# Optimization experiments

Measured on AMD Instinct MI355X. Metric: run time of the kernel, lower is better.

The kernel has to match this reference:

```python
import jax, jax.numpy as jnp
import numpy as np


def setup_inputs() -> dict:
    key = jax.random.key(0)
    k0, k1, k2, k3, k4 = jax.random.split(key, 5)
    c_in, c_feat, c_atten, T = 256, 256, 64, 8
    b, h, w = 8, 64, 64
    return {
        "x": jax.random.normal(k0, (b * T, c_in, h, w), dtype=jnp.float32),
        "W_feat": jax.random.normal(k1, (c_feat, c_in), dtype=jnp.float32) * 0.02,
        "b_feat": jax.random.normal(k2, (c_feat,), dtype=jnp.float32) * 0.02,
        "W_atten": jax.random.normal(k3, (c_atten, c_in), dtype=jnp.float32) * 0.02,
        "b_atten": jax.random.normal(k4, (c_atten,), dtype=jnp.float32) * 0.02,
        "T": T,
    }


def reference(x, W_feat, b_feat, W_atten, b_atten, T):
    bt, c, h, w = x.shape
    b = bt // T
    hw = h * w
    # first frame of each clip: (b, c, h, w)
    x0 = x.reshape(b, T, c, h, w)[:, 0]
    # 1x1 conv == per-pixel matmul over channels
    feat = jnp.einsum('bchw,fc->bfhw', x0, W_feat) + b_feat[None, :, None, None]
    feat = feat.reshape(b, -1, hw)                      # (b, c_feat, hw)
    atten = jnp.einsum('schw,ac->sahw', x, W_atten) + b_atten[None, :, None, None]
    atten = atten.reshape(b, T * W_atten.shape[0], hw)  # (b, T*c_atten, hw)
    atten = jax.nn.softmax(atten, axis=-1)              # softmax over spatial
    context = jnp.einsum('bfs,bas->bfa', feat, atten)   # (b, c_feat, T*c_atten)
    return (context, atten)
```

## Files before the change

kernel.cpp:

```cpp
#include <hip/hip_runtime.h>
#include <hip/hip_bf16.h>

#define HW    4096
#define CIN   256
#define NB    8
#define T_FR  8
#define CTX_ELEMS (NB * 256 * 512)

typedef __attribute__((ext_vector_type(8))) short short8;
typedef __attribute__((ext_vector_type(4))) float f32x4;

__device__ __forceinline__ unsigned short f2bf(float f) {
  union { float f; unsigned int u; } v; v.f = f;
  unsigned int r = v.u + 0x7fffu + ((v.u >> 16) & 1u);
  return (unsigned short)(r >> 16);
}
__device__ __forceinline__ float bf2f(unsigned short u) {
  union { unsigned int u; float f; } v; v.u = ((unsigned int)u) << 16;
  return v.f;
}

#define LROW 264
__global__ __launch_bounds__(256) void k_feat(
    const float* __restrict__ x, const float* __restrict__ Wf,
    const float* __restrict__ bfeat, unsigned short* __restrict__ featbf) {
  const int p0  = blockIdx.x * 128;
  const int f0t = blockIdx.y * 128;
  const int b   = blockIdx.z;
  __shared__ unsigned short Wsh[128 * LROW];
  const int tid = threadIdx.x, lane = tid & 63, wave = tid >> 6;
  {
    const int row = tid >> 1, seg = tid & 1;
    const float* src = Wf + (size_t)(f0t + row) * CIN + seg * 128;
    unsigned short* dst = &Wsh[row * LROW + seg * 128];
#pragma unroll
    for (int i = 0; i < 16; ++i) {
      float4 va = *(const float4*)(src + i * 8);
      float4 vb = *(const float4*)(src + i * 8 + 4);
      short8 w;
      w[0] = (short)f2bf(va.x); w[1] = (short)f2bf(va.y);
      w[2] = (short)f2bf(va.z); w[3] = (short)f2bf(va.w);
      w[4] = (short)f2bf(vb.x); w[5] = (short)f2bf(vb.y);
      w[6] = (short)f2bf(vb.z); w[7] = (short)f2bf(vb.w);
      *(short8*)(dst + i * 8) = w;
    }
  }
  __syncthreads();
  const int r = lane & 15, kg = lane >> 4;
  const int pw = p0 + wave * 32;
  const float* xs = x + (size_t)(b * T_FR) * CIN * HW;
  f32x4 acc[2][8] = {};
  for (int ks = 0; ks < 8; ++ks) {
    short8 afr[2];
#pragma unroll
    for (int mi = 0; mi < 2; ++mi) {
      const float* col = xs + (size_t)(ks * 32 + kg * 8) * HW + pw + mi * 16 + r;
#pragma unroll
      for (int j = 0; j < 8; ++j) afr[mi][j] = (short)f2bf(col[(size_t)j * HW]);
    }
    short8 bfr[8];
#pragma unroll
    for (int nj = 0; nj < 8; ++nj)
      bfr[nj] = *(const short8*)&Wsh[(nj * 16 + r) * LROW + ks * 32 + kg * 8];
#pragma unroll
    for (int mi = 0; mi < 2; ++mi)
#pragma unroll
      for (int nj = 0; nj < 8; ++nj)
        acc[mi][nj] = __builtin_amdgcn_mfma_f32_16x16x32_bf16(afr[mi], bfr[nj], acc[mi][nj], 0, 0, 0);
  }
#pragma unroll
  for (int nj = 0; nj < 8; ++nj) {
    const int f = f0t + nj * 16 + r;
    const float bias = bfeat[f];
#pragma unroll
    for (int mi = 0; mi < 2; ++mi) {
      ushort4 u;
      u.x = f2bf(acc[mi][nj][0] + bias);
      u.y = f2bf(acc[mi][nj][1] + bias);
      u.z = f2bf(acc[mi][nj][2] + bias);
      u.w = f2bf(acc[mi][nj][3] + bias);
      *(ushort4*)&featbf[(size_t)(b * 256 + f) * HW + pw + mi * 16 + kg * 4] = u;
    }
  }
}

__global__ __launch_bounds__(256) void k_att(
    const float* __restrict__ x, const float* __restrict__ Wa,
    const float* __restrict__ batt, unsigned short* __restrict__ attbf,
    float* __restrict__ rsum_part) {
  const int p0 = blockIdx.x * 128;
  const int s  = blockIdx.y;
  __shared__ unsigned short Wsh[64 * LROW];
  __shared__ float wsum[4][64];
  const int tid = threadIdx.x, lane = tid & 63, wave = tid >> 6;
  {
    const int row = tid >> 2, seg = tid & 3;
    const float* src = Wa + (size_t)row * CIN + seg * 64;
    unsigned short* dst = &Wsh[row * LROW + seg * 64];
#pragma unroll
    for (int i = 0; i < 8; ++i) {
      float4 va = *(const float4*)(src + i * 8);
      float4 vb = *(const float4*)(src + i * 8 + 4);
      short8 w;
      w[0] = (short)f2bf(va.x); w[1] = (short)f2bf(va.y);
      w[2] = (short)f2bf(va.z); w[3] = (short)f2bf(va.w);
      w[4] = (short)f2bf(vb.x); w[5] = (short)f2bf(vb.y);
      w[6] = (short)f2bf(vb.z); w[7] = (short)f2bf(vb.w);
      *(short8*)(dst + i * 8) = w;
    }
  }
  __syncthreads();
  const int r = lane & 15, kg = lane >> 4;
  const int pw = p0 + wave * 32;
  const float* xs = x + (size_t)s * CIN * HW;
  f32x4 acc[2][4] = {};
  for (int ks = 0; ks < 8; ++ks) {
    short8 afr[2];
#pragma unroll
    for (int mi = 0; mi < 2; ++mi) {
      const float* col = xs + (size_t)(ks * 32 + kg * 8) * HW + pw + mi * 16 + r;
#pragma unroll
      for (int j = 0; j < 8; ++j) afr[mi][j] = (short)f2bf(col[(size_t)j * HW]);
    }
    short8 bfr[4];
#pragma unroll
    for (int nj = 0; nj < 4; ++nj)
      bfr[nj] = *(const short8*)&Wsh[(nj * 16 + r) * LROW + ks * 32 + kg * 8];
#pragma unroll
    for (int mi = 0; mi < 2; ++mi)
#pragma unroll
      for (int nj = 0; nj < 4; ++nj)
        acc[mi][nj] = __builtin_amdgcn_mfma_f32_16x16x32_bf16(afr[mi], bfr[nj], acc[mi][nj], 0, 0, 0);
  }
  const int b = s >> 3, t = s & 7;
  float rowpart[4];
#pragma unroll
  for (int nj = 0; nj < 4; ++nj) {
    const int a = nj * 16 + r;
    const float bias = batt[a];
    float sp = 0.f;
#pragma unroll
    for (int mi = 0; mi < 2; ++mi) {
      float e0 = __expf(acc[mi][nj][0] + bias);
      float e1 = __expf(acc[mi][nj][1] + bias);
      float e2 = __expf(acc[mi][nj][2] + bias);
      float e3 = __expf(acc[mi][nj][3] + bias);
      sp += e0 + e1 + e2 + e3;
      ushort4 u;
      u.x = f2bf(e0); u.y = f2bf(e1); u.z = f2bf(e2); u.w = f2bf(e3);
      *(ushort4*)&attbf[(size_t)(b * 512 + t * 64 + a) * HW + pw + mi * 16 + kg * 4] = u;
    }
    sp += __shfl_xor(sp, 16);
    sp += __shfl_xor(sp, 32);
    rowpart[nj] = sp;
  }
  if (lane < 16) {
#pragma unroll
    for (int nj = 0; nj < 4; ++nj) wsum[wave][nj * 16 + r] = rowpart[nj];
  }
  __syncthreads();
  if (tid < 64) {
    float tot = wsum[0][tid] + wsum[1][tid] + wsum[2][tid] + wsum[3][tid];
    rsum_part[(size_t)blockIdx.x * 4096 + b * 512 + t * 64 + tid] = tot;
  }
}

__global__ __launch_bounds__(256) void k_rsum(
    const float* __restrict__ rsum_part, float* __restrict__ rsum) {
  const int row = blockIdx.x * 256 + threadIdx.x;
  float s = 0.f;
#pragma unroll
  for (int j = 0; j < 32; ++j) s += rsum_part[(size_t)j * 4096 + row];
  rsum[row] = s;
}

__global__ __launch_bounds__(256) void k_ctx(
    const unsigned short* __restrict__ featbf,
    const unsigned short* __restrict__ attbf,
    float* __restrict__ partial) {
  const int a0 = blockIdx.x * 64;
  const int ft = blockIdx.y;
  const int b  = blockIdx.z >> 3;
  const int kc = blockIdx.z & 7;
  __shared__ unsigned short Bsh[64 * LROW];
  const int tid = threadIdx.x, lane = tid & 63, wave = tid >> 6;
  const int r = lane & 15, kg = lane >> 4;
  const int fbase = ft * 128 + wave * 32;
  const unsigned short* Arow = featbf + (size_t)(b * 256 + fbase + r) * HW + kc * 512 + kg * 8;
  const unsigned short* Bsrc = attbf + (size_t)(b * 512 + a0 + (tid >> 2)) * HW + kc * 512 + (tid & 3) * 64;
  unsigned short* Bdst = &Bsh[(tid >> 2) * LROW + (tid & 3) * 64];
  f32x4 acc[2][4] = {};
  for (int ch = 0; ch < 2; ++ch) {
    __syncthreads();
#pragma unroll
    for (int i = 0; i < 8; ++i)
      *(short8*)(Bdst + i * 8) = *(const short8*)(Bsrc + ch * 256 + i * 8);
    __syncthreads();
#pragma unroll
    for (int ks = 0; ks < 8; ++ks) {
      short8 afr[2];
      afr[0] = *(const short8*)(Arow + ch * 256 + ks * 32);
      afr[1] = *(const short8*)(Arow + ch * 256 + ks * 32 + (size_t)16 * HW);
      short8 bfr[4];
#pragma unroll
      for (int nj = 0; nj < 4; ++nj)
        bfr[nj] = *(const short8*)&Bsh[(nj * 16 + r) * LROW + ks * 32 + kg * 8];
#pragma unroll
      for (int mi = 0; mi < 2; ++mi)
#pragma unroll
        for (int nj = 0; nj < 4; ++nj)
          acc[mi][nj] = __builtin_amdgcn_mfma_f32_16x16x32_bf16(afr[mi], bfr[nj], acc[mi][nj], 0, 0, 0);
    }
  }
  const size_t base = ((size_t)kc << 20) + (size_t)b * (256 * 512);
#pragma unroll
  for (int mi = 0; mi < 2; ++mi)
#pragma unroll
    for (int nj = 0; nj < 4; ++nj)
#pragma unroll
      for (int reg = 0; reg < 4; ++reg) {
        const int f = fbase + mi * 16 + kg * 4 + reg;
        const int a = a0 + nj * 16 + r;
        partial[base + (size_t)f * 512 + a] = acc[mi][nj][reg];
      }
}

__global__ __launch_bounds__(256) void k_ctxred(
    const float* __restrict__ partial, const float* __restrict__ rsum,
    float* __restrict__ ctx) {
  const int idx = blockIdx.x * 256 + threadIdx.x;
  const int a = idx & 511, b = idx >> 17;
  float s = 0.f;
#pragma unroll
  for (int kc = 0; kc < 8; ++kc) s += partial[((size_t)kc << 20) + idx];
  ctx[idx] = s / rsum[b * 512 + a];
}

__global__ __launch_bounds__(256) void k_attn_out(
    const unsigned short* __restrict__ attbf, const float* __restrict__ rsum,
    float* __restrict__ attn) {
  const int row = blockIdx.x;
  const float inv = 1.0f / rsum[row];
  const unsigned short* src = attbf + (size_t)row * HW;
  float* dst = attn + (size_t)row * HW;
  const int tid = threadIdx.x;
#pragma unroll
  for (int i = 0; i < 2; ++i) {
    short8 v = *(const short8*)(src + tid * 8 + i * 2048);
    float4 o0, o1;
    o0.x = bf2f((unsigned short)v[0]) * inv;
    o0.y = bf2f((unsigned short)v[1]) * inv;
    o0.z = bf2f((unsigned short)v[2]) * inv;
    o0.w = bf2f((unsigned short)v[3]) * inv;
    o1.x = bf2f((unsigned short)v[4]) * inv;
    o1.y = bf2f((unsigned short)v[5]) * inv;
    o1.z = bf2f((unsigned short)v[6]) * inv;
    o1.w = bf2f((unsigned short)v[7]) * inv;
    *(float4*)(dst + tid * 8 + i * 2048) = o0;
    *(float4*)(dst + tid * 8 + i * 2048 + 4) = o1;
  }
}

extern "C" void kernel_launch(void* const* d_in, const int* in_sizes, int n_in,
                              void* d_out, int out_size, void* d_ws, size_t ws_size,
                              hipStream_t stream) {
  const float* x     = (const float*)d_in[0];
  const float* Wf    = (const float*)d_in[1];
  const float* bfeat = (const float*)d_in[2];
  const float* Wa    = (const float*)d_in[3];
  const float* ba    = (const float*)d_in[4];
  float* ctx  = (float*)d_out;
  float* attn = ctx + CTX_ELEMS;

  unsigned short* featbf = (unsigned short*)d_ws;
  unsigned short* attbf  = featbf + (size_t)NB * 256 * HW;
  float* rsum_part = (float*)(attbf + (size_t)4096 * HW);
  float* rsum = rsum_part + 32 * 4096;
  float* partial = attn;

  k_feat<<<dim3(32, 2, NB), 256, 0, stream>>>(x, Wf, bfeat, featbf);
  k_att<<<dim3(32, 64), 256, 0, stream>>>(x, Wa, ba, attbf, rsum_part);
  k_rsum<<<16, 256, 0, stream>>>(rsum_part, rsum);
  k_ctx<<<dim3(8, 2, 64), 256, 0, stream>>>(featbf, attbf, partial);
  k_ctxred<<<4096, 256, 0, stream>>>(partial, rsum, ctx);
  k_attn_out<<<4096, 256, 0, stream>>>(attbf, rsum, attn);
}
```

Before: 156.3 us.

## Fuse attention normalization output into context GEMM and halve K-split

The separate k_attn_out pass, which re-read bf16 attention and wrote normalized fp32 attention, is removed. Blocks of the context GEMM with ft==0 now write the normalized attention while staging B tiles into shared memory. The K split drops from 8 to 4 chunks, so there are fewer partial buffers to reduce, and the partial buffers move to the workspace because attn is now written concurrently. The cost is half as many blocks in k_ctx, plus extra global stores in some blocks that may unbalance the work.

```diff
diff --git a/kernel.cpp b/kernel.cpp
--- a/kernel.cpp
+++ b/kernel.cpp
@@ -177,24 +177,46 @@
 __global__ __launch_bounds__(256) void k_ctx(
     const unsigned short* __restrict__ featbf,
     const unsigned short* __restrict__ attbf,
-    float* __restrict__ partial) {
+    const float* __restrict__ rsum,
+    float* __restrict__ partial,
+    float* __restrict__ attn) {
   const int a0 = blockIdx.x * 64;
   const int ft = blockIdx.y;
-  const int b  = blockIdx.z >> 3;
-  const int kc = blockIdx.z & 7;
+  const int b  = blockIdx.z >> 2;
+  const int q  = blockIdx.z & 3;
   __shared__ unsigned short Bsh[64 * LROW];
   const int tid = threadIdx.x, lane = tid & 63, wave = tid >> 6;
   const int r = lane & 15, kg = lane >> 4;
   const int fbase = ft * 128 + wave * 32;
-  const unsigned short* Arow = featbf + (size_t)(b * 256 + fbase + r) * HW + kc * 512 + kg * 8;
-  const unsigned short* Bsrc = attbf + (size_t)(b * 512 + a0 + (tid >> 2)) * HW + kc * 512 + (tid & 3) * 64;
-  unsigned short* Bdst = &Bsh[(tid >> 2) * LROW + (tid & 3) * 64];
+  const int brow = tid >> 2;
+  const int bseg = (tid & 3) * 64;
+  const unsigned short* Arow = featbf + (size_t)(b * 256 + fbase + r) * HW + q * 1024 + kg * 8;
+  const unsigned short* Bsrc = attbf + (size_t)(b * 512 + a0 + brow) * HW + q * 1024 + bseg;
+  unsigned short* Bdst = &Bsh[brow * LROW + bseg];
+  float* attn_row = attn + (size_t)(b * 512 + a0 + brow) * HW + q * 1024 + bseg;
+  const bool wr = (ft == 0);
+  const float inv = 1.0f / rsum[b * 512 + a0 + brow];
   f32x4 acc[2][4] = {};
-  for (int ch = 0; ch < 2; ++ch) {
+  for (int ch = 0; ch < 4; ++ch) {
     __syncthreads();
 #pragma unroll
-    for (int i = 0; i < 8; ++i)
-      *(short8*)(Bdst + i * 8) = *(const short8*)(Bsrc + ch * 256 + i * 8);
+    for (int i = 0; i < 8; ++i) {
+      short8 v = *(const short8*)(Bsrc + ch * 256 + i * 8);
+      *(short8*)(Bdst + i * 8) = v;
+      if (wr) {
+        float4 o0, o1;
+        o0.x = bf2f((unsigned short)v[0]) * inv;
+        o0.y = bf2f((unsigned short)v[1]) * inv;
+        o0.z = bf2f((unsigned short)v[2]) * inv;
+        o0.w = bf2f((unsigned short)v[3]) * inv;
+        o1.x = bf2f((unsigned short)v[4]) * inv;
+        o1.y = bf2f((unsigned short)v[5]) * inv;
+        o1.z = bf2f((unsigned short)v[6]) * inv;
+        o1.w = bf2f((unsigned short)v[7]) * inv;
+        *(float4*)(attn_row + ch * 256 + i * 8) = o0;
+        *(float4*)(attn_row + ch * 256 + i * 8 + 4) = o1;
+      }
+    }
     __syncthreads();
 #pragma unroll
     for (int ks = 0; ks < 8; ++ks) {
@@ -212,7 +234,7 @@
           acc[mi][nj] = __builtin_amdgcn_mfma_f32_16x16x32_bf16(afr[mi], bfr[nj], acc[mi][nj], 0, 0, 0);
     }
   }
-  const size_t base = ((size_t)kc << 20) + (size_t)b * (256 * 512);
+  const size_t base = ((size_t)q << 20) + (size_t)b * (256 * 512);
 #pragma unroll
   for (int mi = 0; mi < 2; ++mi)
 #pragma unroll
@@ -230,35 +252,9 @@
     float* __restrict__ ctx) {
   const int idx = blockIdx.x * 256 + threadIdx.x;
   const int a = idx & 511, b = idx >> 17;
-  float s = 0.f;
-#pragma unroll
-  for (int kc = 0; kc < 8; ++kc) s += partial[((size_t)kc << 20) + idx];
+  float s = partial[idx] + partial[(1 << 20) + idx] +
+            partial[(2 << 20) + idx] + partial[(3 << 20) + idx];
   ctx[idx] = s / rsum[b * 512 + a];
-}
-
-__global__ __launch_bounds__(256) void k_attn_out(
-    const unsigned short* __restrict__ attbf, const float* __restrict__ rsum,
-    float* __restrict__ attn) {
-  const int row = blockIdx.x;
-  const float inv = 1.0f / rsum[row];
-  const unsigned short* src = attbf + (size_t)row * HW;
-  float* dst = attn + (size_t)row * HW;
-  const int tid = threadIdx.x;
-#pragma unroll
-  for (int i = 0; i < 2; ++i) {
-    short8 v = *(const short8*)(src + tid * 8 + i * 2048);
-    float4 o0, o1;
-    o0.x = bf2f((unsigned short)v[0]) * inv;
-    o0.y = bf2f((unsigned short)v[1]) * inv;
-    o0.z = bf2f((unsigned short)v[2]) * inv;
-    o0.w = bf2f((unsigned short)v[3]) * inv;
-    o1.x = bf2f((unsigned short)v[4]) * inv;
-    o1.y = bf2f((unsigned short)v[5]) * inv;
-    o1.z = bf2f((unsigned short)v[6]) * inv;
-    o1.w = bf2f((unsigned short)v[7]) * inv;
-    *(float4*)(dst + tid * 8 + i * 2048) = o0;
-    *(float4*)(dst + tid * 8 + i * 2048 + 4) = o1;
-  }
 }
 
 extern "C" void kernel_launch(void* const* d_in, const int* in_sizes, int n_in,
@@ -276,12 +272,11 @@
   unsigned short* attbf  = featbf + (size_t)NB * 256 * HW;
   float* rsum_part = (float*)(attbf + (size_t)4096 * HW);
   float* rsum = rsum_part + 32 * 4096;
-  float* partial = attn;
+  float* partial = rsum + 4096;
 
   k_feat<<<dim3(32, 2, NB), 256, 0, stream>>>(x, Wf, bfeat, featbf);
   k_att<<<dim3(32, 64), 256, 0, stream>>>(x, Wa, ba, attbf, rsum_part);
   k_rsum<<<16, 256, 0, stream>>>(rsum_part, rsum);
-  k_ctx<<<dim3(8, 2, 64), 256, 0, stream>>>(featbf, attbf, partial);
+  k_ctx<<<dim3(8, 2, 32), 256, 0, stream>>>(featbf, attbf, rsum, partial, attn);
   k_ctxred<<<4096, 256, 0, stream>>>(partial, rsum, ctx);
-  k_attn_out<<<4096, 256, 0, stream>>>(attbf, rsum, attn);
-}
+}
```

New measurement: 178.2 us. +14.0%, slower.

## Retile context GEMM, move partials to workspace, fuse final reduction and attention output

Applied to the files above, without the earlier changes.

The context GEMM now uses blocks covering 32 attention rows by all 256 feature rows over one 512-wide K chunk. The attention tile is loaded once into shared memory and each wave computes 64x32, replacing the two-stage chunk loop. Partial sums now go to a workspace buffer rather than the attention output region, so the ctx reduction and the attention normalization can run together in one combined kernel, saving a launch. The cost is that the feature operand now has many redundant global reads per block and the workspace must be larger. k_att is also launched before k_feat.

```diff
diff --git a/kernel.cpp b/kernel.cpp
--- a/kernel.cpp
+++ b/kernel.cpp
@@ -174,90 +174,89 @@
   rsum[row] = s;
 }
 
+#define BROW 520
 __global__ __launch_bounds__(256) void k_ctx(
     const unsigned short* __restrict__ featbf,
     const unsigned short* __restrict__ attbf,
     float* __restrict__ partial) {
-  const int a0 = blockIdx.x * 64;
-  const int ft = blockIdx.y;
-  const int b  = blockIdx.z >> 3;
-  const int kc = blockIdx.z & 7;
-  __shared__ unsigned short Bsh[64 * LROW];
+  const int a0 = blockIdx.x * 32;
+  const int kc = blockIdx.y;
+  const int b  = blockIdx.z;
+  __shared__ unsigned short Bsh[32 * BROW];
   const int tid = threadIdx.x, lane = tid & 63, wave = tid >> 6;
   const int r = lane & 15, kg = lane >> 4;
-  const int fbase = ft * 128 + wave * 32;
-  const unsigned short* Arow = featbf + (size_t)(b * 256 + fbase + r) * HW + kc * 512 + kg * 8;
-  const unsigned short* Bsrc = attbf + (size_t)(b * 512 + a0 + (tid >> 2)) * HW + kc * 512 + (tid & 3) * 64;
-  unsigned short* Bdst = &Bsh[(tid >> 2) * LROW + (tid & 3) * 64];
-  f32x4 acc[2][4] = {};
-  for (int ch = 0; ch < 2; ++ch) {
-    __syncthreads();
+  {
+    const int row = tid >> 3, seg = tid & 7;
+    const unsigned short* src = attbf + (size_t)(b * 512 + a0 + row) * HW + kc * 512 + seg * 64;
+    unsigned short* dst = &Bsh[row * BROW + seg * 64];
 #pragma unroll
     for (int i = 0; i < 8; ++i)
-      *(short8*)(Bdst + i * 8) = *(const short8*)(Bsrc + ch * 256 + i * 8);
-    __syncthreads();
-#pragma unroll
-    for (int ks = 0; ks < 8; ++ks) {
-      short8 afr[2];
-      afr[0] = *(const short8*)(Arow + ch * 256 + ks * 32);
-      afr[1] = *(const short8*)(Arow + ch * 256 + ks * 32 + (size_t)16 * HW);
-      short8 bfr[4];
-#pragma unroll
-      for (int nj = 0; nj < 4; ++nj)
-        bfr[nj] = *(const short8*)&Bsh[(nj * 16 + r) * LROW + ks * 32 + kg * 8];
-#pragma unroll
-      for (int mi = 0; mi < 2; ++mi)
-#pragma unroll
-        for (int nj = 0; nj < 4; ++nj)
-          acc[mi][nj] = __builtin_amdgcn_mfma_f32_16x16x32_bf16(afr[mi], bfr[nj], acc[mi][nj], 0, 0, 0);
-    }
+      *(short8*)(dst + i * 8) = *(const short8*)(src + i * 8);
+  }
+  __syncthreads();
+  const unsigned short* Arow = featbf + (size_t)(b * 256 + wave * 64 + r) * HW + kc * 512 + kg * 8;
+  f32x4 acc[4][2] = {};
+#pragma unroll
+  for (int ks = 0; ks < 16; ++ks) {
+    short8 afr[4];
+#pragma unroll
+    for (int mi = 0; mi < 4; ++mi)
+      afr[mi] = *(const short8*)(Arow + ks * 32 + (size_t)(mi * 16) * HW);
+    short8 bfr[2];
+#pragma unroll
+    for (int nj = 0; nj < 2; ++nj)
+      bfr[nj] = *(const short8*)&Bsh[(nj * 16 + r) * BROW + ks * 32 + kg * 8];
+#pragma unroll
+    for (int mi = 0; mi < 4; ++mi)
+#pragma unroll
+      for (int nj = 0; nj < 2; ++nj)
+        acc[mi][nj] = __builtin_amdgcn_mfma_f32_16x16x32_bf16(afr[mi], bfr[nj], acc[mi][nj], 0, 0, 0);
   }
   const size_t base = ((size_t)kc << 20) + (size_t)b * (256 * 512);
 #pragma unroll
-  for (int mi = 0; mi < 2; ++mi)
-#pragma unroll
-    for (int nj = 0; nj < 4; ++nj)
+  for (int mi = 0; mi < 4; ++mi)
+#pragma unroll
+    for (int nj = 0; nj < 2; ++nj)
 #pragma unroll
       for (int reg = 0; reg < 4; ++reg) {
-        const int f = fbase + mi * 16 + kg * 4 + reg;
+        const int f = wave * 64 + mi * 16 + kg * 4 + reg;
         const int a = a0 + nj * 16 + r;
         partial[base + (size_t)f * 512 + a] = acc[mi][nj][reg];
       }
 }
 
-__global__ __launch_bounds__(256) void k_ctxred(
+__global__ __launch_bounds__(256) void k_final(
     const float* __restrict__ partial, const float* __restrict__ rsum,
-    float* __restrict__ ctx) {
-  const int idx = blockIdx.x * 256 + threadIdx.x;
-  const int a = idx & 511, b = idx >> 17;
-  float s = 0.f;
-#pragma unroll
-  for (int kc = 0; kc < 8; ++kc) s += partial[((size_t)kc << 20) + idx];
-  ctx[idx] = s / rsum[b * 512 + a];
-}
-
-__global__ __launch_bounds__(256) void k_attn_out(
-    const unsigned short* __restrict__ attbf, const float* __restrict__ rsum,
-    float* __restrict__ attn) {
-  const int row = blockIdx.x;
-  const float inv = 1.0f / rsum[row];
-  const unsigned short* src = attbf + (size_t)row * HW;
-  float* dst = attn + (size_t)row * HW;
-  const int tid = threadIdx.x;
-#pragma unroll
-  for (int i = 0; i < 2; ++i) {
-    short8 v = *(const short8*)(src + tid * 8 + i * 2048);
-    float4 o0, o1;
-    o0.x = bf2f((unsigned short)v[0]) * inv;
-    o0.y = bf2f((unsigned short)v[1]) * inv;
-    o0.z = bf2f((unsigned short)v[2]) * inv;
-    o0.w = bf2f((unsigned short)v[3]) * inv;
-    o1.x = bf2f((unsigned short)v[4]) * inv;
-    o1.y = bf2f((unsigned short)v[5]) * inv;
-    o1.z = bf2f((unsigned short)v[6]) * inv;
-    o1.w = bf2f((unsigned short)v[7]) * inv;
-    *(float4*)(dst + tid * 8 + i * 2048) = o0;
-    *(float4*)(dst + tid * 8 + i * 2048 + 4) = o1;
+    const unsigned short* __restrict__ attbf,
+    float* __restrict__ ctx, float* __restrict__ attn) {
+  if (blockIdx.x < 4096) {
+    const int idx = blockIdx.x * 256 + threadIdx.x;
+    const int a = idx & 511, b = idx >> 17;
+    float s = 0.f;
+#pragma unroll
+    for (int kc = 0; kc < 8; ++kc) s += partial[((size_t)kc << 20) + idx];
+    ctx[idx] = s / rsum[b * 512 + a];
+  } else {
+    const int row = blockIdx.x - 4096;
+    const float inv = 1.0f / rsum[row];
+    const unsigned short* src = attbf + (size_t)row * HW;
+    float* dst = attn + (size_t)row * HW;
+    const int tid = threadIdx.x;
+#pragma unroll
+    for (int i = 0; i < 2; ++i) {
+      short8 v = *(const short8*)(src + tid * 8 + i * 2048);
+      float4 o0, o1;
+      o0.x = bf2f((unsigned short)v[0]) * inv;
+      o0.y = bf2f((unsigned short)v[1]) * inv;
+      o0.z = bf2f((unsigned short)v[2]) * inv;
+      o0.w = bf2f((unsigned short)v[3]) * inv;
+      o1.x = bf2f((unsigned short)v[4]) * inv;
+      o1.y = bf2f((unsigned short)v[5]) * inv;
+      o1.z = bf2f((unsigned short)v[6]) * inv;
+      o1.w = bf2f((unsigned short)v[7]) * inv;
+      *(float4*)(dst + tid * 8 + i * 2048) = o0;
+      *(float4*)(dst + tid * 8 + i * 2048 + 4) = o1;
+    }
   }
 }
 
@@ -276,12 +275,11 @@
   unsigned short* attbf  = featbf + (size_t)NB * 256 * HW;
   float* rsum_part = (float*)(attbf + (size_t)4096 * HW);
   float* rsum = rsum_part + 32 * 4096;
-  float* partial = attn;
-
+  float* partial = rsum + 4096;
+
+  k_att<<<dim3(32, 64), 256, 0, stream>>>(x, Wa, ba, attbf, rsum_part);
   k_feat<<<dim3(32, 2, NB), 256, 0, stream>>>(x, Wf, bfeat, featbf);
-  k_att<<<dim3(32, 64), 256, 0, stream>>>(x, Wa, ba, attbf, rsum_part);
   k_rsum<<<16, 256, 0, stream>>>(rsum_part, rsum);
-  k_ctx<<<dim3(8, 2, 64), 256, 0, stream>>>(featbf, attbf, partial);
-  k_ctxred<<<4096, 256, 0, stream>>>(partial, rsum, ctx);
-  k_attn_out<<<4096, 256, 0, stream>>>(attbf, rsum, attn);
-}
+  k_ctx<<<dim3(16, 8, NB), 256, 0, stream>>>(featbf, attbf, partial);
+  k_final<<<8192, 256, 0, stream>>>(partial, rsum, attbf, ctx, attn);
+}
```

New measurement: 166.6 us. 1.07x slower.

## Merge feat/att GEMM kernels and ctx-reduce/attn-out kernels into combined launches

Applied to the files above, without the earlier changes.

The feature and attention 1x1-conv GEMMs now run as one grid, with blocks dispatched by index. Feature blocks use 64-row tiles, which doubles the feat block count and lets both share the smaller LDS footprint. The context reduction and the attention normalization output are also merged into one kernel, and the context reduce is vectorized to float4. The partial buffer moves from the attn output region into workspace, so the final kernel can write attn while reading partials. The goal is fewer launches and better overlap of tails. The cost is feat blocks re-reading x for each of 4 f-tiles instead of 2, and a larger workspace requirement.

```diff
diff --git a/kernel.cpp b/kernel.cpp
--- a/kernel.cpp
+++ b/kernel.cpp
@@ -21,81 +21,33 @@
 }
 
 #define LROW 264
-__global__ __launch_bounds__(256) void k_feat(
-    const float* __restrict__ x, const float* __restrict__ Wf,
-    const float* __restrict__ bfeat, unsigned short* __restrict__ featbf) {
-  const int p0  = blockIdx.x * 128;
-  const int f0t = blockIdx.y * 128;
-  const int b   = blockIdx.z;
-  __shared__ unsigned short Wsh[128 * LROW];
-  const int tid = threadIdx.x, lane = tid & 63, wave = tid >> 6;
-  {
-    const int row = tid >> 1, seg = tid & 1;
-    const float* src = Wf + (size_t)(f0t + row) * CIN + seg * 128;
-    unsigned short* dst = &Wsh[row * LROW + seg * 128];
-#pragma unroll
-    for (int i = 0; i < 16; ++i) {
-      float4 va = *(const float4*)(src + i * 8);
-      float4 vb = *(const float4*)(src + i * 8 + 4);
-      short8 w;
-      w[0] = (short)f2bf(va.x); w[1] = (short)f2bf(va.y);
-      w[2] = (short)f2bf(va.z); w[3] = (short)f2bf(va.w);
-      w[4] = (short)f2bf(vb.x); w[5] = (short)f2bf(vb.y);
-      w[6] = (short)f2bf(vb.z); w[7] = (short)f2bf(vb.w);
-      *(short8*)(dst + i * 8) = w;
-    }
-  }
-  __syncthreads();
-  const int r = lane & 15, kg = lane >> 4;
-  const int pw = p0 + wave * 32;
-  const float* xs = x + (size_t)(b * T_FR) * CIN * HW;
-  f32x4 acc[2][8] = {};
-  for (int ks = 0; ks < 8; ++ks) {
-    short8 afr[2];
-#pragma unroll
-    for (int mi = 0; mi < 2; ++mi) {
-      const float* col = xs + (size_t)(ks * 32 + kg * 8) * HW + pw + mi * 16 + r;
-#pragma unroll
-      for (int j = 0; j < 8; ++j) afr[mi][j] = (short)f2bf(col[(size_t)j * HW]);
-    }
-    short8 bfr[8];
-#pragma unroll
-    for (int nj = 0; nj < 8; ++nj)
-      bfr[nj] = *(const short8*)&Wsh[(nj * 16 + r) * LROW + ks * 32 + kg * 8];
-#pragma unroll
-    for (int mi = 0; mi < 2; ++mi)
-#pragma unroll
-      for (int nj = 0; nj < 8; ++nj)
-        acc[mi][nj] = __builtin_amdgcn_mfma_f32_16x16x32_bf16(afr[mi], bfr[nj], acc[mi][nj], 0, 0, 0);
-  }
-#pragma unroll
-  for (int nj = 0; nj < 8; ++nj) {
-    const int f = f0t + nj * 16 + r;
-    const float bias = bfeat[f];
-#pragma unroll
-    for (int mi = 0; mi < 2; ++mi) {
-      ushort4 u;
-      u.x = f2bf(acc[mi][nj][0] + bias);
-      u.y = f2bf(acc[mi][nj][1] + bias);
-      u.z = f2bf(acc[mi][nj][2] + bias);
-      u.w = f2bf(acc[mi][nj][3] + bias);
-      *(ushort4*)&featbf[(size_t)(b * 256 + f) * HW + pw + mi * 16 + kg * 4] = u;
-    }
-  }
-}
-
-__global__ __launch_bounds__(256) void k_att(
+__global__ __launch_bounds__(256) void k_main(
     const float* __restrict__ x, const float* __restrict__ Wa,
-    const float* __restrict__ batt, unsigned short* __restrict__ attbf,
-    float* __restrict__ rsum_part) {
-  const int p0 = blockIdx.x * 128;
-  const int s  = blockIdx.y;
+    const float* __restrict__ Wf, const float* __restrict__ batt,
+    const float* __restrict__ bfeat, unsigned short* __restrict__ attbf,
+    unsigned short* __restrict__ featbf, float* __restrict__ rsum_part) {
+  const int bid = blockIdx.x;
   __shared__ unsigned short Wsh[64 * LROW];
   __shared__ float wsum[4][64];
   const int tid = threadIdx.x, lane = tid & 63, wave = tid >> 6;
+
+  const bool is_att = bid < 2048;
+  int pb, s, ftile, b;
+  const float* Wsrc;
+  if (is_att) {
+    pb = bid & 31; s = bid >> 5; ftile = 0; b = 0;
+    Wsrc = Wa;
+  } else {
+    const int fb = bid - 2048;
+    pb = fb & 31;
+    const int g = fb >> 5;
+    ftile = g & 3; b = g >> 2; s = b * T_FR;
+    Wsrc = Wf + (size_t)(ftile * 64) * CIN;
+  }
+
   {
     const int row = tid >> 2, seg = tid & 3;
-    const float* src = Wa + (size_t)row * CIN + seg * 64;
+    const float* src = Wsrc + (size_t)row * CIN + seg * 64;
     unsigned short* dst = &Wsh[row * LROW + seg * 64];
 #pragma unroll
     for (int i = 0; i < 8; ++i) {
@@ -110,8 +62,9 @@
     }
   }
   __syncthreads();
+
   const int r = lane & 15, kg = lane >> 4;
-  const int pw = p0 + wave * 32;
+  const int pw = pb * 128 + wave * 32;
   const float* xs = x + (size_t)s * CIN * HW;
   f32x4 acc[2][4] = {};
   for (int ks = 0; ks < 8; ++ks) {
@@ -132,36 +85,54 @@
       for (int nj = 0; nj < 4; ++nj)
         acc[mi][nj] = __builtin_amdgcn_mfma_f32_16x16x32_bf16(afr[mi], bfr[nj], acc[mi][nj], 0, 0, 0);
   }
-  const int b = s >> 3, t = s & 7;
-  float rowpart[4];
-#pragma unroll
-  for (int nj = 0; nj < 4; ++nj) {
-    const int a = nj * 16 + r;
-    const float bias = batt[a];
-    float sp = 0.f;
-#pragma unroll
-    for (int mi = 0; mi < 2; ++mi) {
-      float e0 = __expf(acc[mi][nj][0] + bias);
-      float e1 = __expf(acc[mi][nj][1] + bias);
-      float e2 = __expf(acc[mi][nj][2] + bias);
-      float e3 = __expf(acc[mi][nj][3] + bias);
-      sp += e0 + e1 + e2 + e3;
-      ushort4 u;
-      u.x = f2bf(e0); u.y = f2bf(e1); u.z = f2bf(e2); u.w = f2bf(e3);
-      *(ushort4*)&attbf[(size_t)(b * 512 + t * 64 + a) * HW + pw + mi * 16 + kg * 4] = u;
-    }
-    sp += __shfl_xor(sp, 16);
-    sp += __shfl_xor(sp, 32);
-    rowpart[nj] = sp;
-  }
-  if (lane < 16) {
-#pragma unroll
-    for (int nj = 0; nj < 4; ++nj) wsum[wave][nj * 16 + r] = rowpart[nj];
-  }
-  __syncthreads();
-  if (tid < 64) {
-    float tot = wsum[0][tid] + wsum[1][tid] + wsum[2][tid] + wsum[3][tid];
-    rsum_part[(size_t)blockIdx.x * 4096 + b * 512 + t * 64 + tid] = tot;
+
+  if (is_att) {
+    const int bb = s >> 3, t = s & 7;
+    float rowpart[4];
+#pragma unroll
+    for (int nj = 0; nj < 4; ++nj) {
+      const int a = nj * 16 + r;
+      const float bias = batt[a];
+      float sp = 0.f;
+#pragma unroll
+      for (int mi = 0; mi < 2; ++mi) {
+        float e0 = __expf(acc[mi][nj][0] + bias);
+        float e1 = __expf(acc[mi][nj][1] + bias);
+        float e2 = __expf(acc[mi][nj][2] + bias);
+        float e3 = __expf(acc[mi][nj][3] + bias);
+        sp += e0 + e1 + e2 + e3;
+        ushort4 u;
+        u.x = f2bf(e0); u.y = f2bf(e1); u.z = f2bf(e2); u.w = f2bf(e3);
+        *(ushort4*)&attbf[(size_t)(bb * 512 + t * 64 + a) * HW + pw + mi * 16 + kg * 4] = u;
+      }
+      sp += __shfl_xor(sp, 16);
+      sp += __shfl_xor(sp, 32);
+      rowpart[nj] = sp;
+    }
+    if (lane < 16) {
+#pragma unroll
+      for (int nj = 0; nj < 4; ++nj) wsum[wave][nj * 16 + r] = rowpart[nj];
+    }
+    __syncthreads();
+    if (tid < 64) {
+      float tot = wsum[0][tid] + wsum[1][tid] + wsum[2][tid] + wsum[3][tid];
+      rsum_part[(size_t)pb * 4096 + bb * 512 + t * 64 + tid] = tot;
+    }
+  } else {
+#pragma unroll
+    for (int nj = 0; nj < 4; ++nj) {
+      const int f = ftile * 64 + nj * 16 + r;
+      const float bias = bfeat[f];
+#pragma unroll
+      for (int mi = 0; mi < 2; ++mi) {
+        ushort4 u;
+        u.x = f2bf(acc[mi][nj][0] + bias);
+        u.y = f2bf(acc[mi][nj][1] + bias);
+        u.z = f2bf(acc[mi][nj][2] + bias);
+        u.w = f2bf(acc[mi][nj][3] + bias);
+        *(ushort4*)&featbf[(size_t)(b * 256 + f) * HW + pw + mi * 16 + kg * 4] = u;
+      }
+    }
   }
 }
 
@@ -225,39 +196,43 @@
       }
 }
 
-__global__ __launch_bounds__(256) void k_ctxred(
+__global__ __launch_bounds__(256) void k_final(
     const float* __restrict__ partial, const float* __restrict__ rsum,
-    float* __restrict__ ctx) {
-  const int idx = blockIdx.x * 256 + threadIdx.x;
-  const int a = idx & 511, b = idx >> 17;
-  float s = 0.f;
-#pragma unroll
-  for (int kc = 0; kc < 8; ++kc) s += partial[((size_t)kc << 20) + idx];
-  ctx[idx] = s / rsum[b * 512 + a];
-}
-
-__global__ __launch_bounds__(256) void k_attn_out(
-    const unsigned short* __restrict__ attbf, const float* __restrict__ rsum,
-    float* __restrict__ attn) {
-  const int row = blockIdx.x;
-  const float inv = 1.0f / rsum[row];
-  const unsigned short* src = attbf + (size_t)row * HW;
-  float* dst = attn + (size_t)row * HW;
-  const int tid = threadIdx.x;
-#pragma unroll
-  for (int i = 0; i < 2; ++i) {
-    short8 v = *(const short8*)(src + tid * 8 + i * 2048);
-    float4 o0, o1;
-    o0.x = bf2f((unsigned short)v[0]) * inv;
-    o0.y = bf2f((unsigned short)v[1]) * inv;
-    o0.z = bf2f((unsigned short)v[2]) * inv;
-    o0.w = bf2f((unsigned short)v[3]) * inv;
-    o1.x = bf2f((unsigned short)v[4]) * inv;
-    o1.y = bf2f((unsigned short)v[5]) * inv;
-    o1.z = bf2f((unsigned short)v[6]) * inv;
-    o1.w = bf2f((unsigned short)v[7]) * inv;
-    *(float4*)(dst + tid * 8 + i * 2048) = o0;
-    *(float4*)(dst + tid * 8 + i * 2048 + 4) = o1;
+    const unsigned short* __restrict__ attbf,
+    float* __restrict__ ctx, float* __restrict__ attn) {
+  if (blockIdx.x < 1024) {
+    const int i4 = (blockIdx.x * 256 + threadIdx.x) * 4;
+    const int a = i4 & 511, b = i4 >> 17;
+    float4 s = *(const float4*)&partial[i4];
+#pragma unroll
+    for (int kc = 1; kc < 8; ++kc) {
+      float4 p = *(const float4*)&partial[((size_t)kc << 20) + i4];
+      s.x += p.x; s.y += p.y; s.z += p.z; s.w += p.w;
+    }
+    const float4 rs = *(const float4*)&rsum[b * 512 + a];
+    s.x /= rs.x; s.y /= rs.y; s.z /= rs.z; s.w /= rs.w;
+    *(float4*)&ctx[i4] = s;
+  } else {
+    const int row = blockIdx.x - 1024;
+    const float inv = 1.0f / rsum[row];
+    const unsigned short* src = attbf + (size_t)row * HW;
+    float* dst = attn + (size_t)row * HW;
+    const int tid = threadIdx.x;
+#pragma unroll
+    for (int i = 0; i < 2; ++i) {
+      short8 v = *(const short8*)(src + tid * 8 + i * 2048);
+      float4 o0, o1;
+      o0.x = bf2f((unsigned short)v[0]) * inv;
+      o0.y = bf2f((unsigned short)v[1]) * inv;
+      o0.z = bf2f((unsigned short)v[2]) * inv;
+      o0.w = bf2f((unsigned short)v[3]) * inv;
+      o1.x = bf2f((unsigned short)v[4]) * inv;
+      o1.y = bf2f((unsigned short)v[5]) * inv;
+      o1.z = bf2f((unsigned short)v[6]) * inv;
+      o1.w = bf2f((unsigned short)v[7]) * inv;
+      *(float4*)(dst + tid * 8 + i * 2048) = o0;
+      *(float4*)(dst + tid * 8 + i * 2048 + 4) = o1;
+    }
   }
 }
 
@@ -276,12 +251,10 @@
   unsigned short* attbf  = featbf + (size_t)NB * 256 * HW;
   float* rsum_part = (float*)(attbf + (size_t)4096 * HW);
   float* rsum = rsum_part + 32 * 4096;
-  float* partial = attn;
-
-  k_feat<<<dim3(32, 2, NB), 256, 0, stream>>>(x, Wf, bfeat, featbf);
-  k_att<<<dim3(32, 64), 256, 0, stream>>>(x, Wa, ba, attbf, rsum_part);
+  float* partial = rsum + 4096;
+
+  k_main<<<3072, 256, 0, stream>>>(x, Wa, Wf, ba, bfeat, attbf, featbf, rsum_part);
   k_rsum<<<16, 256, 0, stream>>>(rsum_part, rsum);
   k_ctx<<<dim3(8, 2, 64), 256, 0, stream>>>(featbf, attbf, partial);
-  k_ctxred<<<4096, 256, 0, stream>>>(partial, rsum, ctx);
-  k_attn_out<<<4096, 256, 0, stream>>>(attbf, rsum, attn);
-}
+  k_final<<<5120, 256, 0, stream>>>(partial, rsum, attbf, ctx, attn);
+}
```

Result: faster. 146.3 us (-6.4%).
